# Kernel tuning notes

Measured on AMD Instinct MI355X. Metric: run time of the kernel, lower is better.

The kernel has to match this reference:

```python
import jax, jax.numpy as jnp
from jax import lax
import numpy as np

# Graph / tensor dims
N = 64          # regular nodes (each has a ResistiveTensor state)
N1 = N + 1      # + virtual input node (original node -1), zero state, source-only
E = 513         # 512 random edges + 1 input edge; each edge has its own Reverb conv
B, C, H, W = 8, 3, 64, 64
K = 4           # Reverb kernel_size
EQ = -0.1       # ResistiveTensor equilibrium


def setup_inputs() -> dict:
    key = jax.random.key(0)
    ks = jax.random.split(key, 7)
    states = jax.random.normal(ks[0], (N1, B, C, H, W), jnp.float32)
    states = states.at[N].set(0.0)  # virtual input node has zero state
    noise = jax.random.normal(ks[1], (N1, B, C, H, W), jnp.float32) * 0.05
    conv_w = jax.random.normal(ks[2], (E, C, C, K, K), jnp.float32) * 0.1
    conv_b = jax.random.normal(ks[3], (E, C), jnp.float32) * 0.01
    resistivity = jax.random.uniform(ks[4], (N, B, C, H, W), jnp.float32)
    src = jax.random.randint(ks[5], (E,), 0, N1)   # sources may include input node N
    dst = jax.random.randint(ks[6], (E,), 0, N)    # targets are regular nodes only
    return dict(states=states, noise=noise, conv_w=conv_w, conv_b=conv_b,
                resistivity=resistivity, src=src, dst=dst)


def _conv_same(x, w, b):
    # x: [B,C,H,W], w: [Cout,Cin,K,K]; even kernel -> asymmetric SAME padding (1,2)
    y = lax.conv_general_dilated(x, w, (1, 1), [(1, 2), (1, 2)],
                                 dimension_numbers=('NCHW', 'OIHW', 'NCHW'))
    return y + b[None, :, None, None]


def reference(states, noise, conv_w, conv_b, resistivity, src, dst):
    # Phase 1: per-node activation (with injected noise), as in time_step
    acts = jax.nn.sigmoid(states + noise)            # [N1,B,C,H,W]
    # Phase 2: per-edge gather -> Reverb conv -> scatter-add into target states
    edge_in = acts[src]                              # [E,B,C,H,W] gather
    updates = jax.vmap(_conv_same)(edge_in, conv_w, conv_b)  # [E,B,C,H,W]
    agg = jax.ops.segment_sum(updates, dst, num_segments=N1)  # scatter-add by target
    # ResistiveTensor accumulate: pull toward equilibrium scaled by |resistivity|
    new_states = states + agg
    new_states = new_states.at[:N].add(jnp.abs(resistivity) * (EQ - states[:N]))
    return new_states
```

## Files before the change

### kernel.cpp

```cpp
#include <hip/hip_runtime.h>

#define NN 64
#define BB 8
#define HH 64
#define WW 64
#define EE 513
#define EQF -0.1f
#define IMG 4096
#define CHW 12288

typedef unsigned short u16;
typedef __attribute__((ext_vector_type(8))) short bf16x8;
typedef __attribute__((ext_vector_type(4))) float f32x4;

#define ROWS_P 67
#define B_STR (ROWS_P * 256)
#define N_STR (BB * B_STR)

#define TROW_B 528
#define TILE_B (19 * TROW_B)
#define NPIECE 608

__device__ __forceinline__ u16 f2bf(float f) {
  union { float f; unsigned u; } c; c.f = f;
  return (u16)((c.u + 0x7fffu + ((c.u >> 16) & 1u)) >> 16);
}

__device__ __forceinline__ void wg_barrier() {
  asm volatile("s_waitcnt lgkmcnt(0)\n\ts_barrier" ::: "memory");
  __builtin_amdgcn_sched_barrier(0);
}

__global__ __launch_bounds__(512) void pre_k(const float* __restrict__ conv_w,
                                             const float* __restrict__ conv_b,
                                             const int* __restrict__ src,
                                             const int* __restrict__ dst,
                                             const float* __restrict__ states,
                                             const float* __restrict__ noise,
                                             u16* __restrict__ actsI,
                                             u16* __restrict__ wfrag,
                                             int* __restrict__ csr_off,
                                             int2* __restrict__ csr2,
                                             float* __restrict__ nodeBias,
                                             int* __restrict__ nodePerm,
                                             float* __restrict__ out) {
  __shared__ int sdst[EE];
  __shared__ int ssrc[EE];
  __shared__ int swcnt[8][64];
  __shared__ int spw[8][64];
  __shared__ int soffs[NN + 1];
  __shared__ int slist[EE];
  const int tid = threadIdx.x;
  const int bid = blockIdx.x;

  if (bid == 0) {
    for (int e = tid; e < EE; e += 512) { sdst[e] = dst[e]; ssrc[e] = src[e]; }
    __syncthreads();
    const int wv = tid >> 6, l = tid & 63;
    const int d = sdst[tid];
    int rank = 0, cnt = 0;
    for (int i = 0; i < 64; ++i) {
      int di = __shfl(d, i, 64);
      rank += (di == d && i < l) ? 1 : 0;
      cnt  += (di == l) ? 1 : 0;
    }
    swcnt[wv][l] = cnt;
    __syncthreads();
    if (tid < 64) {
      int s = 0;
      #pragma unroll
      for (int w2 = 0; w2 < 8; ++w2) { spw[w2][tid] = s; s += swcnt[w2][tid]; }
      int tot = s + ((sdst[512] == tid) ? 1 : 0);
      int scan = tot;
      #pragma unroll
      for (int ofs = 1; ofs < 64; ofs <<= 1) {
        int v = __shfl_up(scan, ofs, 64);
        if (tid >= ofs) scan += v;
      }
      soffs[tid] = scan - tot;
      if (tid == 63) soffs[64] = scan;
      int prank = 0;
      #pragma unroll
      for (int m = 0; m < 64; ++m) {
        int cm = __shfl(tot, m, 64);
        prank += (cm > tot || (cm == tot && m < tid)) ? 1 : 0;
      }
      nodePerm[prank] = tid;
    }
    __syncthreads();
    slist[soffs[d] + spw[wv][d] + rank] = tid;
    if (tid == 0) { int d5 = sdst[512]; slist[soffs[d5 + 1] - 1] = 512; }
    __syncthreads();
    if (tid <= NN) csr_off[tid] = soffs[tid];
    for (int q = tid; q < EE; q += 512) {
      int ee = slist[q];
      csr2[q] = make_int2(ssrc[ee] * N_STR, ee * 512);
    }
    if (tid < 192) {
      int n = tid / 3, co = tid - n * 3;
      float s = 0.f;
      for (int q = soffs[n]; q < soffs[n + 1]; ++q)
        s += conv_b[slist[q] * 3 + co];
      nodeBias[tid] = s;
    }
  } else if (bid <= 65) {
    int gid = (bid - 1) * 512 + tid;
    if (gid < EE * 64) {
      int e = gid >> 6, l = gid & 63;
      int g = l >> 4, col = l & 15, co = col >> 2, kw = col & 3;
      u16 v[8];
      #pragma unroll
      for (int j = 0; j < 8; ++j) {
        float f = 0.0f;
        if (co < 3 && j < 3) f = conv_w[e * 144 + co * 48 + j * 16 + g * 4 + kw];
        v[j] = f2bf(f);
      }
      uint4 pk;
      pk.x = (unsigned)v[0] | ((unsigned)v[1] << 16);
      pk.y = (unsigned)v[2] | ((unsigned)v[3] << 16);
      pk.z = (unsigned)v[4] | ((unsigned)v[5] << 16);
      pk.w = (unsigned)v[6] | ((unsigned)v[7] << 16);
      *(uint4*)(wfrag + (size_t)gid * 8) = pk;
    }
  } else {
    int idx = (bid - 66) * 512 + tid;
    int w4 = idx & 15, h = (idx >> 4) & 63, b = (idx >> 10) & 7, n = idx >> 13;
    int pbase = (n * 8 + b) * CHW + h * 64 + w4 * 4;
    float4 s0 = *(const float4*)(states + pbase);
    float4 s1 = *(const float4*)(states + pbase + IMG);
    float4 s2 = *(const float4*)(states + pbase + 2 * IMG);
    float4 z0 = *(const float4*)(noise + pbase);
    float4 z1 = *(const float4*)(noise + pbase + IMG);
    float4 z2 = *(const float4*)(noise + pbase + 2 * IMG);
    float a0[4], a1[4], a2[4];
    #pragma unroll
    for (int p = 0; p < 4; ++p) {
      float v0 = ((const float*)&s0)[p] + ((const float*)&z0)[p];
      float v1 = ((const float*)&s1)[p] + ((const float*)&z1)[p];
      float v2 = ((const float*)&s2)[p] + ((const float*)&z2)[p];
      a0[p] = 1.0f / (1.0f + __expf(-v0));
      a1[p] = 1.0f / (1.0f + __expf(-v1));
      a2[p] = 1.0f / (1.0f + __expf(-v2));
    }
    uint4 q0, q1;
    q0.x = (unsigned)f2bf(a0[0]) | ((unsigned)f2bf(a1[0]) << 16);
    q0.y = (unsigned)f2bf(a2[0]);
    q0.z = (unsigned)f2bf(a0[1]) | ((unsigned)f2bf(a1[1]) << 16);
    q0.w = (unsigned)f2bf(a2[1]);
    q1.x = (unsigned)f2bf(a0[2]) | ((unsigned)f2bf(a1[2]) << 16);
    q1.y = (unsigned)f2bf(a2[2]);
    q1.z = (unsigned)f2bf(a0[3]) | ((unsigned)f2bf(a1[3]) << 16);
    q1.w = (unsigned)f2bf(a2[3]);
    u16* dp = actsI + (size_t)((n * 8 + b) * ROWS_P + (h + 1)) * 256 + w4 * 16;
    *(uint4*)dp = q0;
    *(uint4*)(dp + 8) = q1;
    uint4 zz; zz.x = 0u; zz.y = 0u; zz.z = 0u; zz.w = 0u;
    if (h == 0) {
      u16* zp = actsI + (size_t)((n * 8 + b) * ROWS_P + 0) * 256 + w4 * 16;
      *(uint4*)zp = zz; *(uint4*)(zp + 8) = zz;
    }
    if (h == 63) {
      u16* zp = actsI + (size_t)((n * 8 + b) * ROWS_P + 65) * 256 + w4 * 16;
      *(uint4*)zp = zz; *(uint4*)(zp + 8) = zz;
      zp += 256;
      *(uint4*)zp = zz; *(uint4*)(zp + 8) = zz;
    }
    if (n == NN) {
      *(float4*)(out + pbase) = s0;
      *(float4*)(out + pbase + IMG) = s1;
      *(float4*)(out + pbase + 2 * IMG) = s2;
    }
  }
}

__global__ __launch_bounds__(256, 3) void conv_k(const float* __restrict__ states,
                                                 const float* __restrict__ res,
                                                 const u16* __restrict__ actsI,
                                                 const u16* __restrict__ wfrag,
                                                 const int* __restrict__ csr_off,
                                                 const int2* __restrict__ csr2,
                                                 const float* __restrict__ nodeBias,
                                                 const int* __restrict__ nodePerm,
                                                 float* __restrict__ out) {
  __shared__ __align__(16) char smem[2 * TILE_B];

  const int tid = threadIdx.x, lane = tid & 63, wid = tid >> 6;
  const int bid = blockIdx.x;
  const int n = nodePerm[bid >> 5];
  const int b = (bid >> 2) & 7, ht = bid & 3;
  const int R0 = ht * 16;

  int pg[3], pl[3];
  #pragma unroll
  for (int j = 0; j < 3; ++j) {
    int p = tid + j * 256;
    int row = p >> 5, c16 = p & 31;
    pg[j] = b * B_STR + (R0 + row) * 256 + c16 * 8;
    pl[j] = row * TROW_B + c16 * 16;
  }
  const bool pv2 = (tid + 512) < NPIECE;

  const int g = lane >> 4, px = lane & 15;
  const int abase = (wid * 4 + g) * TROW_B + px * 8;

  f32x4 acc[4][4];
  #pragma unroll
  for (int wr = 0; wr < 4; ++wr)
    #pragma unroll
    for (int t = 0; t < 4; ++t) { acc[wr][t][0]=0.f; acc[wr][t][1]=0.f; acc[wr][t][2]=0.f; acc[wr][t][3]=0.f; }

  const int e0 = csr_off[n], cnt = csr_off[n + 1] - e0;

  uint4 a0, a1, a2; bf16x8 wa;
  uint4 b0, b1, b2; bf16x8 wb;
  uint4 c0, c1, c2; bf16x8 wc;

#define LOADP(R0_,R1_,R2_,WF_,I_) do {                                        \
    int2 c_ = csr2[e0 + (I_)];                                                \
    int sx_ = __builtin_amdgcn_readfirstlane(c_.x);                           \
    int wx_ = __builtin_amdgcn_readfirstlane(c_.y);                           \
    const u16* ap_ = actsI + sx_;                                             \
    R0_ = *(const uint4*)(ap_ + pg[0]);                                       \
    R1_ = *(const uint4*)(ap_ + pg[1]);                                       \
    if (pv2) R2_ = *(const uint4*)(ap_ + pg[2]);                              \
    WF_ = *(const bf16x8*)(wfrag + wx_ + lane * 8);                           \
  } while (0)

#define STOREP(R0_,R1_,R2_,BOFS_) do {                                        \
    *(uint4*)(smem + (BOFS_) + pl[0]) = R0_;                                  \
    *(uint4*)(smem + (BOFS_) + pl[1]) = R1_;                                  \
    if (pv2) *(uint4*)(smem + (BOFS_) + pl[2]) = R2_;                         \
  } while (0)

#define COMP(BOFS_,WF_) do {                                                  \
    _Pragma("unroll")                                                         \
    for (int wr_ = 0; wr_ < 4; ++wr_) {                                       \
      _Pragma("unroll")                                                       \
      for (int t_ = 0; t_ < 4; ++t_) {                                        \
        short4 d_ = *(const short4*)(smem + (BOFS_) + abase + wr_ * TROW_B + t_ * 128); \
        bf16x8 av_;                                                           \
        av_[0]=d_.x; av_[1]=d_.y; av_[2]=d_.z; av_[3]=d_.w;                   \
        av_[4]=0; av_[5]=0; av_[6]=0; av_[7]=0;                               \
        acc[wr_][t_] = __builtin_amdgcn_mfma_f32_16x16x32_bf16(av_, WF_, acc[wr_][t_], 0, 0, 0); \
      }                                                                       \
    }                                                                         \
  } while (0)

#define PHASE(R0_,R1_,R2_,WF_,NEXTI_) do {                                    \
    STOREP(R0_, R1_, R2_, bofs);                                              \
    bf16x8 wcur_ = WF_;                                                       \
    if ((NEXTI_) < cnt) LOADP(R0_, R1_, R2_, WF_, (NEXTI_));                  \
    wg_barrier();                                                             \
    COMP(bofs, wcur_);                                                        \
    bofs ^= TILE_B;                                                           \
  } while (0)

  if (cnt > 0) LOADP(a0, a1, a2, wa, 0);
  if (cnt > 1) LOADP(b0, b1, b2, wb, 1);
  if (cnt > 2) LOADP(c0, c1, c2, wc, 2);
  int bofs = 0;
  int i = 0;
  for (; i + 2 < cnt; i += 3) {
    PHASE(a0, a1, a2, wa, i + 3);
    PHASE(b0, b1, b2, wb, i + 4);
    PHASE(c0, c1, c2, wc, i + 5);
  }
  if (i < cnt)     PHASE(a0, a1, a2, wa, cnt);
  if (i + 1 < cnt) PHASE(b0, b1, b2, wb, cnt);

  __syncthreads();
  float* zr = (float*)(smem + wid * 3328);
  const float bc0 = nodeBias[n * 3 + 0];
  const float bc1 = nodeBias[n * 3 + 1];
  const float bc2 = nodeBias[n * 3 + 2];
  const int col = lane & 15;
  #pragma unroll
  for (int wr = 0; wr < 4; ++wr) {
    if (col < 12) {
      #pragma unroll
      for (int t = 0; t < 4; ++t)
        #pragma unroll
        for (int r = 0; r < 4; ++r)
          zr[(t * 16 + g * 4 + r) * 13 + col] = acc[wr][t][r];
    }
    int hr = R0 + wid * 4 + wr;
    #pragma unroll
    for (int co = 0; co < 3; ++co) {
      float y = (co == 0) ? bc0 : ((co == 1) ? bc1 : bc2);
      #pragma unroll
      for (int kw = 0; kw < 4; ++kw) {
        int wp = lane + kw - 1;
        if (wp >= 0 && wp < 64) y += zr[wp * 13 + co * 4 + kw];
      }
      int o = ((n * 8 + b) * 3 + co) * IMG + hr * 64 + lane;
      float st = states[o];
      out[o] = st + fabsf(res[o]) * (EQF - st) + y;
    }
  }
}

extern "C" void kernel_launch(void* const* d_in, const int* in_sizes, int n_in,
                              void* d_out, int out_size, void* d_ws, size_t ws_size,
                              hipStream_t stream) {
  const float* states = (const float*)d_in[0];
  const float* noise  = (const float*)d_in[1];
  const float* conv_w = (const float*)d_in[2];
  const float* conv_b = (const float*)d_in[3];
  const float* res    = (const float*)d_in[4];
  const int*   src    = (const int*)d_in[5];
  const int*   dst    = (const int*)d_in[6];
  float* out = (float*)d_out;

  u16* actsI = (u16*)d_ws;
  u16* wfrag = (u16*)((char*)d_ws + 17838080);
  int* csr_off = (int*)((char*)d_ws + 18363392);
  int2* csr2 = (int2*)((char*)d_ws + 18363712);
  float* nodeBias = (float*)((char*)d_ws + 18367816);
  int* nodePerm = (int*)((char*)d_ws + 18368584);

  pre_k<<<1106, 512, 0, stream>>>(conv_w, conv_b, src, dst, states, noise,
                                  actsI, wfrag, csr_off, csr2, nodeBias, nodePerm, out);
  conv_k<<<2048, 256, 0, stream>>>(states, res, actsI, wfrag, csr_off, csr2,
                                   nodeBias, nodePerm, out);
}
```

Measured before the change: 58.59 us.

## Halve conv tile height, double blocks, move resistive update into pre kernel

The conv kernel now handles 8-row tiles instead of 16, which doubles the grid to 4096 blocks and shrinks LDS and accumulator use so occupancy can rise to 5 blocks per CU. The load pipeline drops from three-deep to two-deep register prefetch. The resistive equilibrium term (states + |res|*(EQ-states)) is now computed in pre_k and written to out, and conv_k only does out += y. This removes the states/res reads from the conv epilogue at the cost of a read-modify-write of out and more halo overlap per tile (11 rows loaded for 8 output rows).

```diff
diff --git a/kernel.cpp b/kernel.cpp
--- a/kernel.cpp
+++ b/kernel.cpp
@@ -18,8 +18,8 @@
 #define N_STR (BB * B_STR)
 
 #define TROW_B 528
-#define TILE_B (19 * TROW_B)
-#define NPIECE 608
+#define TILE_B (11 * TROW_B)
+#define NPIECE 352
 
 __device__ __forceinline__ u16 f2bf(float f) {
   union { float f; unsigned u; } c; c.f = f;
@@ -37,6 +37,7 @@
                                              const int* __restrict__ dst,
                                              const float* __restrict__ states,
                                              const float* __restrict__ noise,
+                                             const float* __restrict__ res,
                                              u16* __restrict__ actsI,
                                              u16* __restrict__ wfrag,
                                              int* __restrict__ csr_off,
@@ -169,104 +170,110 @@
       *(float4*)(out + pbase) = s0;
       *(float4*)(out + pbase + IMG) = s1;
       *(float4*)(out + pbase + 2 * IMG) = s2;
+    } else {
+      float4 r0 = *(const float4*)(res + pbase);
+      float4 r1 = *(const float4*)(res + pbase + IMG);
+      float4 r2 = *(const float4*)(res + pbase + 2 * IMG);
+      float4 o0, o1, o2;
+      #pragma unroll
+      for (int p = 0; p < 4; ++p) {
+        ((float*)&o0)[p] = ((const float*)&s0)[p] + fabsf(((const float*)&r0)[p]) * (EQF - ((const float*)&s0)[p]);
+        ((float*)&o1)[p] = ((const float*)&s1)[p] + fabsf(((const float*)&r1)[p]) * (EQF - ((const float*)&s1)[p]);
+        ((float*)&o2)[p] = ((const float*)&s2)[p] + fabsf(((const float*)&r2)[p]) * (EQF - ((const float*)&s2)[p]);
+      }
+      *(float4*)(out + pbase) = o0;
+      *(float4*)(out + pbase + IMG) = o1;
+      *(float4*)(out + pbase + 2 * IMG) = o2;
     }
   }
 }
 
-__global__ __launch_bounds__(256, 3) void conv_k(const float* __restrict__ states,
-                                                 const float* __restrict__ res,
-                                                 const u16* __restrict__ actsI,
+__global__ __launch_bounds__(256, 5) void conv_k(const u16* __restrict__ actsI,
                                                  const u16* __restrict__ wfrag,
                                                  const int* __restrict__ csr_off,
                                                  const int2* __restrict__ csr2,
                                                  const float* __restrict__ nodeBias,
                                                  const int* __restrict__ nodePerm,
                                                  float* __restrict__ out) {
-  __shared__ __align__(16) char smem[2 * TILE_B];
+  __shared__ __align__(16) char smem[13312];
 
   const int tid = threadIdx.x, lane = tid & 63, wid = tid >> 6;
   const int bid = blockIdx.x;
-  const int n = nodePerm[bid >> 5];
-  const int b = (bid >> 2) & 7, ht = bid & 3;
-  const int R0 = ht * 16;
-
-  int pg[3], pl[3];
+  const int n = nodePerm[bid >> 6];
+  const int b = (bid >> 3) & 7, ht = bid & 7;
+  const int R0 = ht * 8;
+
+  int pg[2], pl[2];
   #pragma unroll
-  for (int j = 0; j < 3; ++j) {
+  for (int j = 0; j < 2; ++j) {
     int p = tid + j * 256;
     int row = p >> 5, c16 = p & 31;
     pg[j] = b * B_STR + (R0 + row) * 256 + c16 * 8;
     pl[j] = row * TROW_B + c16 * 16;
   }
-  const bool pv2 = (tid + 512) < NPIECE;
+  const bool pv1 = tid < (NPIECE - 256);
 
   const int g = lane >> 4, px = lane & 15;
-  const int abase = (wid * 4 + g) * TROW_B + px * 8;
-
-  f32x4 acc[4][4];
+  const int abase = (wid * 2 + g) * TROW_B + px * 8;
+
+  f32x4 acc[2][4];
   #pragma unroll
-  for (int wr = 0; wr < 4; ++wr)
+  for (int h2 = 0; h2 < 2; ++h2)
     #pragma unroll
-    for (int t = 0; t < 4; ++t) { acc[wr][t][0]=0.f; acc[wr][t][1]=0.f; acc[wr][t][2]=0.f; acc[wr][t][3]=0.f; }
+    for (int t = 0; t < 4; ++t) { acc[h2][t][0]=0.f; acc[h2][t][1]=0.f; acc[h2][t][2]=0.f; acc[h2][t][3]=0.f; }
 
   const int e0 = csr_off[n], cnt = csr_off[n + 1] - e0;
 
-  uint4 a0, a1, a2; bf16x8 wa;
-  uint4 b0, b1, b2; bf16x8 wb;
-  uint4 c0, c1, c2; bf16x8 wc;
-
-#define LOADP(R0_,R1_,R2_,WF_,I_) do {                                        \
+  uint4 a0, a1; bf16x8 wa;
+  uint4 b0, b1; bf16x8 wb;
+
+#define LOADP(R0_,R1_,WF_,I_) do {                                            \
     int2 c_ = csr2[e0 + (I_)];                                                \
     int sx_ = __builtin_amdgcn_readfirstlane(c_.x);                           \
     int wx_ = __builtin_amdgcn_readfirstlane(c_.y);                           \
     const u16* ap_ = actsI + sx_;                                             \
     R0_ = *(const uint4*)(ap_ + pg[0]);                                       \
-    R1_ = *(const uint4*)(ap_ + pg[1]);                                       \
-    if (pv2) R2_ = *(const uint4*)(ap_ + pg[2]);                              \
+    if (pv1) R1_ = *(const uint4*)(ap_ + pg[1]);                              \
     WF_ = *(const bf16x8*)(wfrag + wx_ + lane * 8);                           \
   } while (0)
 
-#define STOREP(R0_,R1_,R2_,BOFS_) do {                                        \
+#define STOREP(R0_,R1_,BOFS_) do {                                            \
     *(uint4*)(smem + (BOFS_) + pl[0]) = R0_;                                  \
-    *(uint4*)(smem + (BOFS_) + pl[1]) = R1_;                                  \
-    if (pv2) *(uint4*)(smem + (BOFS_) + pl[2]) = R2_;                         \
+    if (pv1) *(uint4*)(smem + (BOFS_) + pl[1]) = R1_;                         \
   } while (0)
 
 #define COMP(BOFS_,WF_) do {                                                  \
     _Pragma("unroll")                                                         \
-    for (int wr_ = 0; wr_ < 4; ++wr_) {                                       \
+    for (int h2_ = 0; h2_ < 2; ++h2_) {                                       \
       _Pragma("unroll")                                                       \
       for (int t_ = 0; t_ < 4; ++t_) {                                        \
-        short4 d_ = *(const short4*)(smem + (BOFS_) + abase + wr_ * TROW_B + t_ * 128); \
+        short4 d_ = *(const short4*)(smem + (BOFS_) + abase + h2_ * TROW_B + t_ * 128); \
         bf16x8 av_;                                                           \
         av_[0]=d_.x; av_[1]=d_.y; av_[2]=d_.z; av_[3]=d_.w;                   \
         av_[4]=0; av_[5]=0; av_[6]=0; av_[7]=0;                               \
-        acc[wr_][t_] = __builtin_amdgcn_mfma_f32_16x16x32_bf16(av_, WF_, acc[wr_][t_], 0, 0, 0); \
+        acc[h2_][t_] = __builtin_amdgcn_mfma_f32_16x16x32_bf16(av_, WF_, acc[h2_][t_], 0, 0, 0); \
       }                                                                       \
     }                                                                         \
   } while (0)
 
-#define PHASE(R0_,R1_,R2_,WF_,NEXTI_) do {                                    \
-    STOREP(R0_, R1_, R2_, bofs);                                              \
+#define PHASE(R0_,R1_,WF_,NEXTI_) do {                                        \
+    STOREP(R0_, R1_, bofs);                                                   \
     bf16x8 wcur_ = WF_;                                                       \
-    if ((NEXTI_) < cnt) LOADP(R0_, R1_, R2_, WF_, (NEXTI_));                  \
+    if ((NEXTI_) < cnt) LOADP(R0_, R1_, WF_, (NEXTI_));                       \
     wg_barrier();                                                             \
     COMP(bofs, wcur_);                                                        \
     bofs ^= TILE_B;                                                           \
   } while (0)
 
-  if (cnt > 0) LOADP(a0, a1, a2, wa, 0);
-  if (cnt > 1) LOADP(b0, b1, b2, wb, 1);
-  if (cnt > 2) LOADP(c0, c1, c2, wc, 2);
+  if (cnt > 0) LOADP(a0, a1, wa, 0);
+  if (cnt > 1) LOADP(b0, b1, wb, 1);
   int bofs = 0;
   int i = 0;
-  for (; i + 2 < cnt; i += 3) {
-    PHASE(a0, a1, a2, wa, i + 3);
-    PHASE(b0, b1, b2, wb, i + 4);
-    PHASE(c0, c1, c2, wc, i + 5);
+  for (; i + 1 < cnt; i += 2) {
+    PHASE(a0, a1, wa, i + 2);
+    PHASE(b0, b1, wb, i + 3);
   }
-  if (i < cnt)     PHASE(a0, a1, a2, wa, cnt);
-  if (i + 1 < cnt) PHASE(b0, b1, b2, wb, cnt);
+  if (i < cnt) PHASE(a0, a1, wa, cnt);
 
   __syncthreads();
   float* zr = (float*)(smem + wid * 3328);
@@ -275,15 +282,15 @@
   const float bc2 = nodeBias[n * 3 + 2];
   const int col = lane & 15;
   #pragma unroll
-  for (int wr = 0; wr < 4; ++wr) {
+  for (int h2 = 0; h2 < 2; ++h2) {
     if (col < 12) {
       #pragma unroll
       for (int t = 0; t < 4; ++t)
         #pragma unroll
         for (int r = 0; r < 4; ++r)
-          zr[(t * 16 + g * 4 + r) * 13 + col] = acc[wr][t][r];
-    }
-    int hr = R0 + wid * 4 + wr;
+          zr[(t * 16 + g * 4 + r) * 13 + col] = acc[h2][t][r];
+    }
+    int hr = R0 + wid * 2 + h2;
     #pragma unroll
     for (int co = 0; co < 3; ++co) {
       float y = (co == 0) ? bc0 : ((co == 1) ? bc1 : bc2);
@@ -293,8 +300,7 @@
         if (wp >= 0 && wp < 64) y += zr[wp * 13 + co * 4 + kw];
       }
       int o = ((n * 8 + b) * 3 + co) * IMG + hr * 64 + lane;
-      float st = states[o];
-      out[o] = st + fabsf(res[o]) * (EQF - st) + y;
+      out[o] += y;
     }
   }
 }
@@ -318,8 +324,7 @@
   float* nodeBias = (float*)((char*)d_ws + 18367816);
   int* nodePerm = (int*)((char*)d_ws + 18368584);
 
-  pre_k<<<1106, 512, 0, stream>>>(conv_w, conv_b, src, dst, states, noise,
+  pre_k<<<1106, 512, 0, stream>>>(conv_w, conv_b, src, dst, states, noise, res,
                                   actsI, wfrag, csr_off, csr2, nodeBias, nodePerm, out);
-  conv_k<<<2048, 256, 0, stream>>>(states, res, actsI, wfrag, csr_off, csr2,
-                                   nodeBias, nodePerm, out);
-}
+  conv_k<<<4096, 256, 0, stream>>>(actsI, wfrag, csr_off, csr2, nodeBias, nodePerm, out);
+}
```

New measurement: 55.30 us. 5.6% less time.
